# Kernel optimization log

Hardware: AMD Instinct MI355X
Metric: run time of the kernel (lower is better)

The kernel has to match this reference:

```python
import jax, jax.numpy as jnp
import numpy as np

CODEBOOK_SIZE = 4096
DIM = 64


def setup_inputs() -> dict:
    key = jax.random.key(0)
    kx, ke = jax.random.split(key)
    x = jax.random.normal(kx, (8, 4096, DIM), dtype=jnp.float32)
    embed = jax.random.normal(ke, (CODEBOOK_SIZE, DIM), dtype=jnp.float32)  # codebook [K, d]
    return {"x": x, "embed": embed}


def reference(x, embed):
    # Eval-mode forward of EuclideanCodebook (svq_temp=None -> argmax).
    shape = x.shape
    flatten = x.reshape(-1, shape[-1])            # [N, d]
    embed_sq = jnp.sum(embed * embed, axis=-1)    # [K]
    # dist = 2 * x @ embed.T - ||embed||^2  (negative squared distance up to a const in x)
    dist = 2.0 * jnp.matmul(flatten, embed.T) - embed_sq[None, :]  # [N, K]
    embed_ind = jnp.argmax(dist, axis=-1)         # [N]
    embed_ind = embed_ind.reshape(shape[:-1])     # [...]
    quantize = embed[embed_ind]                   # gather -> [..., d]
    return (quantize, embed_ind)
```

## Files before the change

### kernel.cpp

```cpp
#include <hip/hip_runtime.h>
#include <math.h>

#define N_ROWS 32768
#define K_CODES 4096
#define DIM 64
#define SPLITS 4
#define TILES_TOTAL (K_CODES / 32)
#define TILES_PER_SPLIT (TILES_TOTAL / SPLITS)
#define PHASES (TILES_PER_SPLIT / 2)
#define QUANT_ELEMS (N_ROWS * DIM)

typedef _Float16 half8 __attribute__((ext_vector_type(8)));
typedef float floatx16 __attribute__((ext_vector_type(16)));

__device__ __forceinline__ void gld16(const void* g, void* l) {
    __builtin_amdgcn_global_load_lds(
        (const __attribute__((address_space(1))) unsigned int*)g,
        (__attribute__((address_space(3))) unsigned int*)l, 16, 0, 0);
}

__global__ void prep_kernel(const float* __restrict__ embed,
                            float* __restrict__ sq, half8* __restrict__ ehi,
                            half8* __restrict__ elo) {
    __shared__ float part[256];
    const int tid = threadIdx.x;
    const int t = blockIdx.x * 256 + tid;
    const int l = t & 63;
    const int s = (t >> 6) & 3;
    const int c = blockIdx.x;
    const int col = l & 31;
    const int code = c * 32 + col;
    const int koff = (l >> 5) * 8 + 16 * s;
    const float* src = embed + (size_t)code * DIM + koff;
    half8 h, lo;
    float ss = 0.f;
#pragma unroll
    for (int j = 0; j < 8; ++j) {
        float v = src[j];
        ss = fmaf(v, v, ss);
        _Float16 hi = (_Float16)v;
        h[j] = hi;
        lo[j] = (_Float16)(v - (float)hi);
    }
    ehi[t] = h;
    elo[t] = lo;
    part[tid] = ss;
    __syncthreads();
    if (tid < 32) {
        float a = 0.f;
#pragma unroll
        for (int q = 0; q < 8; ++q) a += part[tid + 32 * (q & 1) + 64 * (q >> 1)];
        sq[c * 32 + tid] = a;
    }
}

#define SUBTILE(LH, LL, NSQ, CIDX)                                            \
    {                                                                         \
        const half8* lh = (const half8*)(LH);                                 \
        const half8* ll = (const half8*)(LL);                                 \
        floatx16 acc;                                                         \
        _Pragma("unroll") for (int r = 0; r < 16; ++r) acc[r] = (NSQ);        \
        half8 b;                                                              \
        __builtin_amdgcn_s_setprio(1);                                        \
        b = lh[lane];                                                         \
        acc = __builtin_amdgcn_mfma_f32_32x32x16_f16(ah[0], b, acc, 0, 0, 0); \
        acc = __builtin_amdgcn_mfma_f32_32x32x16_f16(al[0], b, acc, 0, 0, 0); \
        b = lh[64 + lane];                                                    \
        acc = __builtin_amdgcn_mfma_f32_32x32x16_f16(ah[1], b, acc, 0, 0, 0); \
        acc = __builtin_amdgcn_mfma_f32_32x32x16_f16(al[1], b, acc, 0, 0, 0); \
        b = lh[128 + lane];                                                   \
        acc = __builtin_amdgcn_mfma_f32_32x32x16_f16(ah[2], b, acc, 0, 0, 0); \
        acc = __builtin_amdgcn_mfma_f32_32x32x16_f16(al[2], b, acc, 0, 0, 0); \
        b = lh[192 + lane];                                                   \
        acc = __builtin_amdgcn_mfma_f32_32x32x16_f16(ah[3], b, acc, 0, 0, 0); \
        acc = __builtin_amdgcn_mfma_f32_32x32x16_f16(al[3], b, acc, 0, 0, 0); \
        b = ll[lane];                                                         \
        acc = __builtin_amdgcn_mfma_f32_32x32x16_f16(ah[0], b, acc, 0, 0, 0); \
        b = ll[64 + lane];                                                    \
        acc = __builtin_amdgcn_mfma_f32_32x32x16_f16(ah[1], b, acc, 0, 0, 0); \
        b = ll[128 + lane];                                                   \
        acc = __builtin_amdgcn_mfma_f32_32x32x16_f16(ah[2], b, acc, 0, 0, 0); \
        b = ll[192 + lane];                                                   \
        acc = __builtin_amdgcn_mfma_f32_32x32x16_f16(ah[3], b, acc, 0, 0, 0); \
        __builtin_amdgcn_s_setprio(0);                                        \
        const int cidx = (CIDX);                                              \
        _Pragma("unroll") for (int r = 0; r < 16; ++r) {                      \
            if (acc[r] > best[r]) {    \
                best[r] = acc[r];                                             \
                bidx[r] = cidx;                                               \
            }                                                                 \
        }                                                                     \
    }

__global__ __launch_bounds__(256, 4) void fused_dist_argmax32(
    const float* __restrict__ x, const float* __restrict__ sq,
    const half8* __restrict__ ehi, const half8* __restrict__ elo,
    float* __restrict__ pbest, int* __restrict__ pidx) {
    __shared__ __align__(16) char lbuf[2][16384];
    const int tid = threadIdx.x;
    const int lane = tid & 63;
    const int wave = tid >> 6;
    const int col = lane & 31;
    const int half_ = lane >> 5;
    const int row_base = blockIdx.x * 128 + wave * 32;
    const int split = blockIdx.y;
    const int c0 = split * TILES_PER_SPLIT;

    half8 ah[4], al[4];
    {
        const float* xs = x + (size_t)(row_base + col) * DIM + half_ * 8;
#pragma unroll
        for (int s = 0; s < 4; ++s) {
            half8 h, lo;
#pragma unroll
            for (int j = 0; j < 8; ++j) {
                float v = 2.0f * xs[16 * s + j];
                _Float16 hi = (_Float16)v;
                h[j] = hi;
                lo[j] = (_Float16)(v - (float)hi);
            }
            ah[s] = h;
            al[s] = lo;
        }
    }

    float best[16];
    int bidx[16];
#pragma unroll
    for (int r = 0; r < 16; ++r) {
        best[r] = -INFINITY;
        bidx[r] = 0;
    }

    const char* gh = (const char*)(ehi + (size_t)c0 * 256);
    const char* gl = (const char*)(elo + (size_t)c0 * 256);
    const float* psq = sq + c0 * 32 + col;

    {
        char* d = lbuf[0];
        gld16(gh + (size_t)tid * 16, d + tid * 16);
        gld16(gl + (size_t)tid * 16, d + 4096 + tid * 16);
        gld16(gh + 4096 + (size_t)tid * 16, d + 8192 + tid * 16);
        gld16(gl + 4096 + (size_t)tid * 16, d + 12288 + tid * 16);
    }
    float nsqA = -psq[0];
    float nsqB = -psq[32];
    asm volatile("s_waitcnt vmcnt(0)" ::: "memory");
    __builtin_amdgcn_s_barrier();
    asm volatile("" ::: "memory");

    for (int p = 0; p < PHASES; ++p) {
        char* bufc = lbuf[p & 1];
        if (p + 1 < PHASES) {
            char* bufn = lbuf[(p & 1) ^ 1];
            const size_t go = (size_t)(2 * p + 2) * 4096;
            gld16(gh + go + (size_t)tid * 16, bufn + tid * 16);
            gld16(gl + go + (size_t)tid * 16, bufn + 4096 + tid * 16);
            gld16(gh + go + 4096 + (size_t)tid * 16, bufn + 8192 + tid * 16);
            gld16(gl + go + 4096 + (size_t)tid * 16, bufn + 12288 + tid * 16);
        }
        const float nsq0 = nsqA, nsq1 = nsqB;
        if (p + 1 < PHASES) {
            nsqA = -psq[(2 * p + 2) * 32];
            nsqB = -psq[(2 * p + 3) * 32];
        }

        SUBTILE(bufc, bufc + 4096, nsq0, (c0 + 2 * p) * 32 + col);
        SUBTILE(bufc + 8192, bufc + 12288, nsq1, (c0 + 2 * p + 1) * 32 + col);

        asm volatile("s_waitcnt vmcnt(0)" ::: "memory");
        __builtin_amdgcn_s_barrier();
        asm volatile("" ::: "memory");
    }

#pragma unroll
    for (int r = 0; r < 16; ++r) {
        float bv = best[r];
        int bi = bidx[r];
#pragma unroll
        for (int d = 1; d < 32; d <<= 1) {
            float ov = __shfl_xor(bv, d);
            int oi = __shfl_xor(bi, d);
            if (ov > bv || (ov == bv && oi < bi)) {
                bv = ov;
                bi = oi;
            }
        }
        if (col == 0) {
            const int row = row_base + (r & 3) + 8 * (r >> 2) + 4 * half_;
            pbest[(size_t)split * N_ROWS + row] = bv;
            pidx[(size_t)split * N_ROWS + row] = bi;
        }
    }
}

__global__ void combine_kernel(const float* __restrict__ pbest,
                               const int* __restrict__ pidx,
                               const float* __restrict__ embed,
                               float* __restrict__ out) {
    const int t = blockIdx.x * blockDim.x + threadIdx.x;
    const int row = t >> 4;
    const int q = t & 15;
    if (row >= N_ROWS) return;

    float best = -INFINITY;
    int bi = 0;
#pragma unroll
    for (int s = 0; s < SPLITS; ++s) {
        float b = pbest[(size_t)s * N_ROWS + row];
        int i = pidx[(size_t)s * N_ROWS + row];
        if (b > best) {
            best = b;
            bi = i;
        }
    }

    const float4* e4 = reinterpret_cast<const float4*>(embed);
    float4 v = e4[(size_t)bi * (DIM / 4) + q];
    reinterpret_cast<float4*>(out)[(size_t)row * (DIM / 4) + q] = v;
    if (q == 0) {
        out[(size_t)QUANT_ELEMS + row] = (float)bi;
    }
}

extern "C" void kernel_launch(void* const* d_in, const int* in_sizes, int n_in,
                              void* d_out, int out_size, void* d_ws,
                              size_t ws_size, hipStream_t stream) {
    const float* x = (const float*)d_in[0];
    const float* embed = (const float*)d_in[1];
    float* out = (float*)d_out;

    char* ws = (char*)d_ws;
    float* sq = (float*)ws;
    half8* ehi = (half8*)(ws + 16384);
    half8* elo = (half8*)(ws + 16384 + 524288);
    float* pbest = (float*)(ws + 16384 + 2 * 524288);
    int* pidx = (int*)(ws + 16384 + 2 * 524288 + SPLITS * N_ROWS * 4);

    prep_kernel<<<TILES_TOTAL, 256, 0, stream>>>(embed, sq, ehi, elo);

    dim3 grid(N_ROWS / 128, SPLITS);
    fused_dist_argmax32<<<grid, 256, 0, stream>>>(x, sq, ehi, elo, pbest,
                                                  pidx);

    const int combine_threads = N_ROWS * (DIM / 4);
    combine_kernel<<<(combine_threads + 255) / 256, 256, 0, stream>>>(
        pbest, pidx, embed, out);
}
```

Measured before the change: 123.3 us.

## Process 64 rows per wave with two accumulators to reuse codebook fragments

Each wave now handles two 32-row groups, keeping two MFMA accumulators and reusing each codebook B fragment loaded from LDS for both groups. This halves the LDS reads and global codebook traffic per row, and the two independent accumulator chains interleave to hide MFMA dependency latency. The cost is roughly double the register use for x fragments and best/index state, so launch bounds drop to 2 blocks per CU and the grid halves, which lowers occupancy.

```diff
diff --git a/kernel.cpp b/kernel.cpp
--- a/kernel.cpp
+++ b/kernel.cpp
@@ -58,41 +58,60 @@
     {                                                                         \
         const half8* lh = (const half8*)(LH);                                 \
         const half8* ll = (const half8*)(LL);                                 \
-        floatx16 acc;                                                         \
-        _Pragma("unroll") for (int r = 0; r < 16; ++r) acc[r] = (NSQ);        \
+        floatx16 a0, a1;                                                      \
+        _Pragma("unroll") for (int r = 0; r < 16; ++r) {                      \
+            a0[r] = (NSQ);                                                    \
+            a1[r] = (NSQ);                                                    \
+        }                                                                     \
         half8 b;                                                              \
         __builtin_amdgcn_s_setprio(1);                                        \
         b = lh[lane];                                                         \
-        acc = __builtin_amdgcn_mfma_f32_32x32x16_f16(ah[0], b, acc, 0, 0, 0); \
-        acc = __builtin_amdgcn_mfma_f32_32x32x16_f16(al[0], b, acc, 0, 0, 0); \
+        a0 = __builtin_amdgcn_mfma_f32_32x32x16_f16(ah[0], b, a0, 0, 0, 0);   \
+        a1 = __builtin_amdgcn_mfma_f32_32x32x16_f16(ah[4], b, a1, 0, 0, 0);   \
+        a0 = __builtin_amdgcn_mfma_f32_32x32x16_f16(al[0], b, a0, 0, 0, 0);   \
+        a1 = __builtin_amdgcn_mfma_f32_32x32x16_f16(al[4], b, a1, 0, 0, 0);   \
         b = lh[64 + lane];                                                    \
-        acc = __builtin_amdgcn_mfma_f32_32x32x16_f16(ah[1], b, acc, 0, 0, 0); \
-        acc = __builtin_amdgcn_mfma_f32_32x32x16_f16(al[1], b, acc, 0, 0, 0); \
+        a0 = __builtin_amdgcn_mfma_f32_32x32x16_f16(ah[1], b, a0, 0, 0, 0);   \
+        a1 = __builtin_amdgcn_mfma_f32_32x32x16_f16(ah[5], b, a1, 0, 0, 0);   \
+        a0 = __builtin_amdgcn_mfma_f32_32x32x16_f16(al[1], b, a0, 0, 0, 0);   \
+        a1 = __builtin_amdgcn_mfma_f32_32x32x16_f16(al[5], b, a1, 0, 0, 0);   \
         b = lh[128 + lane];                                                   \
-        acc = __builtin_amdgcn_mfma_f32_32x32x16_f16(ah[2], b, acc, 0, 0, 0); \
-        acc = __builtin_amdgcn_mfma_f32_32x32x16_f16(al[2], b, acc, 0, 0, 0); \
+        a0 = __builtin_amdgcn_mfma_f32_32x32x16_f16(ah[2], b, a0, 0, 0, 0);   \
+        a1 = __builtin_amdgcn_mfma_f32_32x32x16_f16(ah[6], b, a1, 0, 0, 0);   \
+        a0 = __builtin_amdgcn_mfma_f32_32x32x16_f16(al[2], b, a0, 0, 0, 0);   \
+        a1 = __builtin_amdgcn_mfma_f32_32x32x16_f16(al[6], b, a1, 0, 0, 0);   \
         b = lh[192 + lane];                                                   \
-        acc = __builtin_amdgcn_mfma_f32_32x32x16_f16(ah[3], b, acc, 0, 0, 0); \
-        acc = __builtin_amdgcn_mfma_f32_32x32x16_f16(al[3], b, acc, 0, 0, 0); \
+        a0 = __builtin_amdgcn_mfma_f32_32x32x16_f16(ah[3], b, a0, 0, 0, 0);   \
+        a1 = __builtin_amdgcn_mfma_f32_32x32x16_f16(ah[7], b, a1, 0, 0, 0);   \
+        a0 = __builtin_amdgcn_mfma_f32_32x32x16_f16(al[3], b, a0, 0, 0, 0);   \
+        a1 = __builtin_amdgcn_mfma_f32_32x32x16_f16(al[7], b, a1, 0, 0, 0);   \
         b = ll[lane];                                                         \
-        acc = __builtin_amdgcn_mfma_f32_32x32x16_f16(ah[0], b, acc, 0, 0, 0); \
+        a0 = __builtin_amdgcn_mfma_f32_32x32x16_f16(ah[0], b, a0, 0, 0, 0);   \
+        a1 = __builtin_amdgcn_mfma_f32_32x32x16_f16(ah[4], b, a1, 0, 0, 0);   \
         b = ll[64 + lane];                                                    \
-        acc = __builtin_amdgcn_mfma_f32_32x32x16_f16(ah[1], b, acc, 0, 0, 0); \
+        a0 = __builtin_amdgcn_mfma_f32_32x32x16_f16(ah[1], b, a0, 0, 0, 0);   \
+        a1 = __builtin_amdgcn_mfma_f32_32x32x16_f16(ah[5], b, a1, 0, 0, 0);   \
         b = ll[128 + lane];                                                   \
-        acc = __builtin_amdgcn_mfma_f32_32x32x16_f16(ah[2], b, acc, 0, 0, 0); \
+        a0 = __builtin_amdgcn_mfma_f32_32x32x16_f16(ah[2], b, a0, 0, 0, 0);   \
+        a1 = __builtin_amdgcn_mfma_f32_32x32x16_f16(ah[6], b, a1, 0, 0, 0);   \
         b = ll[192 + lane];                                                   \
-        acc = __builtin_amdgcn_mfma_f32_32x32x16_f16(ah[3], b, acc, 0, 0, 0); \
+        a0 = __builtin_amdgcn_mfma_f32_32x32x16_f16(ah[3], b, a0, 0, 0, 0);   \
+        a1 = __builtin_amdgcn_mfma_f32_32x32x16_f16(ah[7], b, a1, 0, 0, 0);   \
         __builtin_amdgcn_s_setprio(0);                                        \
         const int cidx = (CIDX);                                              \
         _Pragma("unroll") for (int r = 0; r < 16; ++r) {                      \
-            if (acc[r] > best[r]) {    \
-                best[r] = acc[r];                                             \
+            if (a0[r] > best[r]) {     \
+                best[r] = a0[r];                                              \
                 bidx[r] = cidx;                                               \
             }                                                                 \
+            if (a1[r] > best[16 + r]) {                                       \
+                best[16 + r] = a1[r];                                         \
+                bidx[16 + r] = cidx;                                          \
+            }                                                                 \
         }                                                                     \
     }
 
-__global__ __launch_bounds__(256, 4) void fused_dist_argmax32(
+__global__ __launch_bounds__(256, 2) void fused_dist_argmax64(
     const float* __restrict__ x, const float* __restrict__ sq,
     const half8* __restrict__ ehi, const half8* __restrict__ elo,
     float* __restrict__ pbest, int* __restrict__ pidx) {
@@ -102,13 +121,15 @@
     const int wave = tid >> 6;
     const int col = lane & 31;
     const int half_ = lane >> 5;
-    const int row_base = blockIdx.x * 128 + wave * 32;
+    const int row_base = blockIdx.x * 256 + wave * 64;
     const int split = blockIdx.y;
     const int c0 = split * TILES_PER_SPLIT;
 
-    half8 ah[4], al[4];
-    {
-        const float* xs = x + (size_t)(row_base + col) * DIM + half_ * 8;
+    half8 ah[8], al[8];
+#pragma unroll
+    for (int g = 0; g < 2; ++g) {
+        const float* xs =
+            x + (size_t)(row_base + g * 32 + col) * DIM + half_ * 8;
 #pragma unroll
         for (int s = 0; s < 4; ++s) {
             half8 h, lo;
@@ -119,15 +140,15 @@
                 h[j] = hi;
                 lo[j] = (_Float16)(v - (float)hi);
             }
-            ah[s] = h;
-            al[s] = lo;
-        }
-    }
-
-    float best[16];
-    int bidx[16];
-#pragma unroll
-    for (int r = 0; r < 16; ++r) {
+            ah[g * 4 + s] = h;
+            al[g * 4 + s] = lo;
+        }
+    }
+
+    float best[32];
+    int bidx[32];
+#pragma unroll
+    for (int r = 0; r < 32; ++r) {
         best[r] = -INFINITY;
         bidx[r] = 0;
     }
@@ -174,7 +195,7 @@
     }
 
 #pragma unroll
-    for (int r = 0; r < 16; ++r) {
+    for (int r = 0; r < 32; ++r) {
         float bv = best[r];
         int bi = bidx[r];
 #pragma unroll
@@ -187,7 +208,9 @@
             }
         }
         if (col == 0) {
-            const int row = row_base + (r & 3) + 8 * (r >> 2) + 4 * half_;
+            const int rr = r & 15;
+            const int row = row_base + (r >> 4) * 32 + (rr & 3) + 8 * (rr >> 2) +
+                            4 * half_;
             pbest[(size_t)split * N_ROWS + row] = bv;
             pidx[(size_t)split * N_ROWS + row] = bi;
         }
@@ -239,8 +262,8 @@
 
     prep_kernel<<<TILES_TOTAL, 256, 0, stream>>>(embed, sq, ehi, elo);
 
-    dim3 grid(N_ROWS / 128, SPLITS);
-    fused_dist_argmax32<<<grid, 256, 0, stream>>>(x, sq, ehi, elo, pbest,
+    dim3 grid(N_ROWS / 256, SPLITS);
+    fused_dist_argmax64<<<grid, 256, 0, stream>>>(x, sq, ehi, elo, pbest,
                                                   pidx);
 
     const int combine_threads = N_ROWS * (DIM / 4);
```

After: 124.7 us. Within noise of the previous version (+1.1%).

## Merge split argmax via packed 64-bit atomicMax and stagger block starts

Applied to the files above, without the earlier changes.

Each block now folds its per-row best into a single order-preserving 64-bit key (mapped float score in the high bits, inverted index in the low bits) using atomicMax, instead of writing per-split partial best/index arrays. The combine kernel then reads one key per row. prep_kernel zeroes the key buffer, which works because every valid key compares above zero. It also adds an s_sleep stagger at block start to spread out initial memory bursts, at the cost of a small fixed delay and atomic contention from the 4 splits hitting each row.

```diff
diff --git a/kernel.cpp b/kernel.cpp
--- a/kernel.cpp
+++ b/kernel.cpp
@@ -21,10 +21,12 @@
 
 __global__ void prep_kernel(const float* __restrict__ embed,
                             float* __restrict__ sq, half8* __restrict__ ehi,
-                            half8* __restrict__ elo) {
+                            half8* __restrict__ elo,
+                            unsigned long long* __restrict__ keys) {
     __shared__ float part[256];
     const int tid = threadIdx.x;
     const int t = blockIdx.x * 256 + tid;
+    keys[t] = 0ull;
     const int l = t & 63;
     const int s = (t >> 6) & 3;
     const int c = blockIdx.x;
@@ -53,6 +55,73 @@
         sq[c * 32 + tid] = a;
     }
 }
+
+__global__ __launch_bounds__(256, 4) void fused_dist_argmax32(
+    const float* __restrict__ x, const float* __restrict__ sq,
+    const half8* __restrict__ ehi, const half8* __restrict__ elo,
+    unsigned long long* __restrict__ keys) {
+    __shared__ __align__(16) char lbuf[2][16384];
+
+    {
+        const int stag = (blockIdx.x + blockIdx.y) & 3;
+        if (stag > 0) __builtin_amdgcn_s_sleep(15);
+        if (stag > 1) __builtin_amdgcn_s_sleep(15);
+        if (stag > 2) __builtin_amdgcn_s_sleep(15);
+    }
+
+    const int tid = threadIdx.x;
+    const int lane = tid & 63;
+    const int wave = tid >> 6;
+    const int col = lane & 31;
+    const int half_ = lane >> 5;
+    const int row_base = blockIdx.x * 128 + wave * 32;
+    const int split = blockIdx.y;
+    const int c0 = split * TILES_PER_SPLIT;
+
+    half8 ah[4], al[4];
+    {
+        const float* xs = x + (size_t)(row_base + col) * DIM + half_ * 8;
+#pragma unroll
+        for (int s = 0; s < 4; ++s) {
+            half8 h, lo;
+#pragma unroll
+            for (int j = 0; j < 8; ++j) {
+                float v = 2.0f * xs[16 * s + j];
+                _Float16 hi = (_Float16)v;
+                h[j] = hi;
+                lo[j] = (_Float16)(v - (float)hi);
+            }
+            ah[s] = h;
+            al[s] = lo;
+        }
+    }
+
+    float best[16];
+    int bidx[16];
+#pragma unroll
+    for (int r = 0; r < 16; ++r) {
+        best[r] = -INFINITY;
+        bidx[r] = 0;
+    }
+
+    const char* gh = (const char*)(ehi + (size_t)c0 * 256);
+    const char* gl = (const char*)(elo + (size_t)c0 * 256);
+    const float* psq = sq + c0 * 32 + col;
+    const half8* lh0 = (const half8*)lbuf[0];
+    const half8* ll0 = (const half8*)(lbuf[0] + 4096);
+
+    {
+        char* d = lbuf[0];
+        gld16(gh + (size_t)tid * 16, d + tid * 16);
+        gld16(gl + (size_t)tid * 16, d + 4096 + tid * 16);
+        gld16(gh + 4096 + (size_t)tid * 16, d + 8192 + tid * 16);
+        gld16(gl + 4096 + (size_t)tid * 16, d + 12288 + tid * 16);
+    }
+    float nsqA = -psq[0];
+    float nsqB = -psq[32];
+    asm volatile("s_waitcnt vmcnt(0)" ::: "memory");
+    __builtin_amdgcn_s_barrier();
+    asm volatile("" ::: "memory");
 
 #define SUBTILE(LH, LL, NSQ, CIDX)                                            \
     {                                                                         \
@@ -92,63 +161,6 @@
         }                                                                     \
     }
 
-__global__ __launch_bounds__(256, 4) void fused_dist_argmax32(
-    const float* __restrict__ x, const float* __restrict__ sq,
-    const half8* __restrict__ ehi, const half8* __restrict__ elo,
-    float* __restrict__ pbest, int* __restrict__ pidx) {
-    __shared__ __align__(16) char lbuf[2][16384];
-    const int tid = threadIdx.x;
-    const int lane = tid & 63;
-    const int wave = tid >> 6;
-    const int col = lane & 31;
-    const int half_ = lane >> 5;
-    const int row_base = blockIdx.x * 128 + wave * 32;
-    const int split = blockIdx.y;
-    const int c0 = split * TILES_PER_SPLIT;
-
-    half8 ah[4], al[4];
-    {
-        const float* xs = x + (size_t)(row_base + col) * DIM + half_ * 8;
-#pragma unroll
-        for (int s = 0; s < 4; ++s) {
-            half8 h, lo;
-#pragma unroll
-            for (int j = 0; j < 8; ++j) {
-                float v = 2.0f * xs[16 * s + j];
-                _Float16 hi = (_Float16)v;
-                h[j] = hi;
-                lo[j] = (_Float16)(v - (float)hi);
-            }
-            ah[s] = h;
-            al[s] = lo;
-        }
-    }
-
-    float best[16];
-    int bidx[16];
-#pragma unroll
-    for (int r = 0; r < 16; ++r) {
-        best[r] = -INFINITY;
-        bidx[r] = 0;
-    }
-
-    const char* gh = (const char*)(ehi + (size_t)c0 * 256);
-    const char* gl = (const char*)(elo + (size_t)c0 * 256);
-    const float* psq = sq + c0 * 32 + col;
-
-    {
-        char* d = lbuf[0];
-        gld16(gh + (size_t)tid * 16, d + tid * 16);
-        gld16(gl + (size_t)tid * 16, d + 4096 + tid * 16);
-        gld16(gh + 4096 + (size_t)tid * 16, d + 8192 + tid * 16);
-        gld16(gl + 4096 + (size_t)tid * 16, d + 12288 + tid * 16);
-    }
-    float nsqA = -psq[0];
-    float nsqB = -psq[32];
-    asm volatile("s_waitcnt vmcnt(0)" ::: "memory");
-    __builtin_amdgcn_s_barrier();
-    asm volatile("" ::: "memory");
-
     for (int p = 0; p < PHASES; ++p) {
         char* bufc = lbuf[p & 1];
         if (p + 1 < PHASES) {
@@ -188,14 +200,17 @@
         }
         if (col == 0) {
             const int row = row_base + (r & 3) + 8 * (r >> 2) + 4 * half_;
-            pbest[(size_t)split * N_ROWS + row] = bv;
-            pidx[(size_t)split * N_ROWS + row] = bi;
-        }
-    }
-}
-
-__global__ void combine_kernel(const float* __restrict__ pbest,
-                               const int* __restrict__ pidx,
+            unsigned ub = __float_as_uint(bv);
+            unsigned mapped = ub ^ (((int)ub >> 31) | 0x80000000u);
+            unsigned long long key =
+                ((unsigned long long)mapped << 32) | (unsigned)(~bi);
+            atomicMax(keys + row, key);
+        }
+    }
+#undef SUBTILE
+}
+
+__global__ void combine_kernel(const unsigned long long* __restrict__ keys,
                                const float* __restrict__ embed,
                                float* __restrict__ out) {
     const int t = blockIdx.x * blockDim.x + threadIdx.x;
@@ -203,17 +218,8 @@
     const int q = t & 15;
     if (row >= N_ROWS) return;
 
-    float best = -INFINITY;
-    int bi = 0;
-#pragma unroll
-    for (int s = 0; s < SPLITS; ++s) {
-        float b = pbest[(size_t)s * N_ROWS + row];
-        int i = pidx[(size_t)s * N_ROWS + row];
-        if (b > best) {
-            best = b;
-            bi = i;
-        }
-    }
+    const unsigned long long key = keys[row];
+    const int bi = (int)(~(unsigned)key);
 
     const float4* e4 = reinterpret_cast<const float4*>(embed);
     float4 v = e4[(size_t)bi * (DIM / 4) + q];
@@ -234,16 +240,15 @@
     float* sq = (float*)ws;
     half8* ehi = (half8*)(ws + 16384);
     half8* elo = (half8*)(ws + 16384 + 524288);
-    float* pbest = (float*)(ws + 16384 + 2 * 524288);
-    int* pidx = (int*)(ws + 16384 + 2 * 524288 + SPLITS * N_ROWS * 4);
-
-    prep_kernel<<<TILES_TOTAL, 256, 0, stream>>>(embed, sq, ehi, elo);
+    unsigned long long* keys =
+        (unsigned long long*)(ws + 16384 + 2 * 524288);
+
+    prep_kernel<<<TILES_TOTAL, 256, 0, stream>>>(embed, sq, ehi, elo, keys);
 
     dim3 grid(N_ROWS / 128, SPLITS);
-    fused_dist_argmax32<<<grid, 256, 0, stream>>>(x, sq, ehi, elo, pbest,
-                                                  pidx);
+    fused_dist_argmax32<<<grid, 256, 0, stream>>>(x, sq, ehi, elo, keys);
 
     const int combine_threads = N_ROWS * (DIM / 4);
     combine_kernel<<<(combine_threads + 255) / 256, 256, 0, stream>>>(
-        pbest, pidx, embed, out);
-}
+        keys, embed, out);
+}
```

Result: no change. 123.3 us (-0.0%).
